# Kernel tuning notes

Measured on AMD Instinct MI355X. Metric: run time of the kernel, lower is better.

## Reference

```python
import jax, jax.numpy as jnp
import numpy as np

Q = 128      # number of slices
S = 8        # slice_length = C // Q = 1024 // 128
H = 32       # unit_dim[0]
BN_EPS = 1e-3  # Keras BatchNormalization default epsilon


def setup_inputs() -> dict:
    key = jax.random.key(0)
    ks = jax.random.split(key, 5)
    B = 32768
    x = jax.random.normal(ks[0], (B, 1, 1, Q * S), dtype=jnp.float32)
    # Per-slice (grouped) parameters for the q=128 independent MLPs.
    W1 = jax.random.normal(ks[1], (Q, S, H), dtype=jnp.float32) / np.sqrt(S)
    b1 = jnp.zeros((Q, H), dtype=jnp.float32)
    gamma = jnp.ones((Q, H), dtype=jnp.float32)
    beta = jnp.zeros((Q, H), dtype=jnp.float32)
    mov_mean = 0.1 * jax.random.normal(ks[2], (Q, H), dtype=jnp.float32)
    mov_var = jnp.ones((Q, H), dtype=jnp.float32) + 0.1 * jax.random.uniform(ks[3], (Q, H), dtype=jnp.float32)
    W2 = jax.random.normal(ks[4], (Q, H, 1), dtype=jnp.float32) / np.sqrt(H)
    b2 = jnp.zeros((Q, 1), dtype=jnp.float32)
    return {"x": x, "W1": W1, "b1": b1, "gamma": gamma, "beta": beta,
            "mov_mean": mov_mean, "mov_var": mov_var, "W2": W2, "b2": b2}


def reference(x, W1, b1, gamma, beta, mov_mean, mov_var, W2, b2):
    B = x.shape[0]
    xs = x.reshape(B, Q, -1)                       # (B, Q, S)
    # Grouped Dense(32) + ELU, all 128 slices in one batched matmul
    h = jnp.einsum('bqs,qsh->bqh', xs, W1) + b1    # (B, Q, H)
    h = jax.nn.elu(h)
    # BatchNormalization (inference: moving statistics)
    inv = gamma * jax.lax.rsqrt(mov_var + BN_EPS)  # (Q, H)
    h = (h - mov_mean) * inv + beta
    # Grouped Dense(1)
    out = jnp.einsum('bqh,qho->bqo', h, W2) + b2   # (B, Q, 1)
    return out[..., 0]                              # (B, Q)
```

## Files before the change

kernel.cpp:

```cpp
#include <hip/hip_runtime.h>
#include <hip/hip_bf16.h>


#define QN 128
#define SN 8
#define HN 32
#define XROW 1024
#define BN_EPS 1e-3f

typedef short bf16x8 __attribute__((ext_vector_type(8)));
typedef float f32x16 __attribute__((ext_vector_type(16)));
typedef unsigned int u32;

#define WS_A_BYTES (QN * 64 * 16)
#define WS_C_OFF   WS_A_BYTES
#define WS_C_BYTES (QN * 32 * 4)
#define WS_W_OFF   (WS_C_OFF + WS_C_BYTES)
#define WS_W_BYTES (QN * 32 * 4)
#define WS_B2_OFF  (WS_W_OFF + WS_W_BYTES)

static __device__ __forceinline__ u32 pkbf(float lo, float hi) {
    union { __hip_bfloat162 h2; u32 u; } c;
    c.h2 = __float22bfloat162_rn(float2{lo, hi});
    return c.u;
}

__global__ void divenc_prep(const float* __restrict__ W1, const float* __restrict__ b1,
                            const float* __restrict__ gamma_, const float* __restrict__ beta_,
                            const float* __restrict__ mmean, const float* __restrict__ mvar,
                            const float* __restrict__ W2, const float* __restrict__ b2,
                            unsigned char* __restrict__ ws)
{
    const int q = blockIdx.x;
    const int m = threadIdx.x;

    u32 d0 = 0, d1 = 0, d2 = 0, d3 = 0;
    if (m < 32) {
        d0 = pkbf(W1[(q*SN + 0)*HN + m], W1[(q*SN + 1)*HN + m]);
        d1 = pkbf(W1[(q*SN + 2)*HN + m], W1[(q*SN + 3)*HN + m]);
        d2 = pkbf(W1[(q*SN + 4)*HN + m], W1[(q*SN + 5)*HN + m]);
        d3 = pkbf(W1[(q*SN + 6)*HN + m], W1[(q*SN + 7)*HN + m]);
    }
    ((uint4*)ws)[q*64 + m] = uint4{d0, d1, d2, d3};

    float* wsC  = (float*)(ws + WS_C_OFF);
    float* wsW  = (float*)(ws + WS_W_OFF);
    float* wsB2 = (float*)(ws + WS_B2_OFF);
    if (m < 32) {
        const int half = m >> 4, r = m & 15;
        const int h = (r & 3) + 8*(r >> 2) + 4*half;
        wsC[q*32 + m] = b1[q*HN + h];
        float inv = gamma_[q*HN+h] * rsqrtf(mvar[q*HN+h] + BN_EPS);
        wsW[q*32 + m] = inv * W2[q*HN + h];
    }
    if (m == 0) {
        float acc = b2[q];
        for (int h = 0; h < HN; ++h) {
            float inv = gamma_[q*HN+h] * rsqrtf(mvar[q*HN+h] + BN_EPS);
            acc += (beta_[q*HN+h] - mmean[q*HN+h]*inv) * W2[q*HN+h];
        }
        wsB2[q] = acc;
    }
}

__global__ __launch_bounds__(512, 4)
void divenc_mfma(const float* __restrict__ x, const unsigned char* __restrict__ ws,
                 float* __restrict__ out)
{
    const int lane = threadIdx.x & 63;
    const int wv   = threadIdx.x >> 6;
    const int half = lane >> 5;
    const int bl   = lane & 31;
    const int b0   = blockIdx.x * 128;
    const int q0   = blockIdx.y * 32;

    const uint4* wsA  = (const uint4*)ws;
    const float* wsC  = (const float*)(ws + WS_C_OFF);
    const float* wsW  = (const float*)(ws + WS_W_OFF);
    const float* wsB2 = (const float*)(ws + WS_B2_OFF);

    __shared__ float slab[2][128][9];

    #pragma unroll
    for (int qg = 0; qg < 4; ++qg) {
        const int q = q0 + qg*8 + wv;

        union { uint4 u; bf16x8 v; } A1, A2;
        A1.u = wsA[q*64 + lane];
        A2.u = wsA[q*64 + (lane ^ 32)];

        f32x16 cini;
        const float* cp_ = wsC + q*32 + half*16;
        #pragma unroll
        for (int r = 0; r < 16; ++r) cini[r] = cp_[r];
        float w2r[16];
        const float* wp_ = wsW + q*32 + half*16;
        #pragma unroll
        for (int r = 0; r < 16; ++r) w2r[r] = wp_[r];
        const float b2p = wsB2[q];

        const float* xq = x + (size_t)b0 * XROW + q * SN;
        float4 xa = *(const float4*)(xq + (size_t)lane * XROW);
        float4 xc = *(const float4*)(xq + (size_t)lane * XROW + 4);

        #pragma unroll
        for (int sub = 0; sub < 2; ++sub) {
            const int nsub = (sub < 1) ? sub + 1 : sub;
            const float* np = xq + (size_t)(nsub*64 + lane) * XROW;
            float4 na = *(const float4*)np;
            float4 nc = *(const float4*)(np + 4);

            union { uint4 u; bf16x8 v; } B;
            B.u = uint4{ pkbf(xa.x, xa.y), pkbf(xa.z, xa.w),
                         pkbf(xc.x, xc.y), pkbf(xc.z, xc.w) };

            f32x16 D0 = __builtin_amdgcn_mfma_f32_32x32x16_bf16(A1.v, B.v, cini, 0, 0, 0);
            f32x16 D1 = __builtin_amdgcn_mfma_f32_32x32x16_bf16(A2.v, B.v, cini, 0, 0, 0);

            float p0 = 0.f, p1 = 0.f;
            #pragma unroll
            for (int r = 0; r < 16; ++r) {
                float z0 = D0[r];
                float e0 = __expf(fminf(z0, 0.f)) - 1.f;
                p0 = fmaf(fmaxf(z0, e0), w2r[r], p0);
                float z1 = D1[r];
                float e1 = __expf(fminf(z1, 0.f)) - 1.f;
                p1 = fmaf(fmaxf(z1, e1), w2r[r], p1);
            }
            p0 += __shfl_xor(p0, 32);
            p1 += __shfl_xor(p1, 32);

            const float v = (half ? p1 : p0) + b2p;
            slab[qg & 1][sub*64 + half*32 + bl][wv] = v;

            xa = na; xc = nc;
        }

        __syncthreads();
        {
            const int row = threadIdx.x >> 2;
            const int cp  = (threadIdx.x & 3) * 2;
            float2 vv;
            vv.x = slab[qg & 1][row][cp + 0];
            vv.y = slab[qg & 1][row][cp + 1];
            *(float2*)(out + (size_t)(b0 + row) * QN + q0 + qg*8 + cp) = vv;
        }
    }
}

extern "C" void kernel_launch(void* const* d_in, const int* in_sizes, int n_in,
                              void* d_out, int out_size, void* d_ws, size_t ws_size,
                              hipStream_t stream) {
    const float* x      = (const float*)d_in[0];
    const float* W1     = (const float*)d_in[1];
    const float* b1     = (const float*)d_in[2];
    const float* gamma_ = (const float*)d_in[3];
    const float* beta_  = (const float*)d_in[4];
    const float* mmean  = (const float*)d_in[5];
    const float* mvar   = (const float*)d_in[6];
    const float* W2     = (const float*)d_in[7];
    const float* b2     = (const float*)d_in[8];
    float* out = (float*)d_out;
    unsigned char* ws = (unsigned char*)d_ws;

    const int Btot = in_sizes[0] / XROW;

    divenc_prep<<<QN, 64, 0, stream>>>(W1, b1, gamma_, beta_, mmean, mvar, W2, b2, ws);
    divenc_mfma<<<dim3(Btot / 128, QN / 32), 512, 0, stream>>>(x, ws, out);
}
```

Before: 58.49 us.

## Stage x tiles into LDS with async double-buffered global_load_lds and swizzle

The kernel now copies x into shared memory with global_load_lds in 32-row chunks, double-buffered so the next chunk loads while the current one is computed. Each row segment covers 16 slices (512 contiguous bytes), so reads are coalesced instead of 32-byte strided per-lane loads. An XOR swizzle keeps LDS reads free of bank conflicts. Each wave now issues one MFMA per slice rather than two, and the grid uses 16 slices per block, doubling the block count. The risks are barrier overhead per chunk and relying on the compiler to wait for the LDS DMA to finish before the barrier.

```diff
diff --git a/kernel.cpp b/kernel.cpp
--- a/kernel.cpp
+++ b/kernel.cpp
@@ -7,10 +7,15 @@
 #define HN 32
 #define XROW 1024
 #define BN_EPS 1e-3f
+#define ROWS_BLK 128
+#define QBLK 16
 
 typedef short bf16x8 __attribute__((ext_vector_type(8)));
 typedef float f32x16 __attribute__((ext_vector_type(16)));
 typedef unsigned int u32;
+
+typedef __attribute__((address_space(1))) void as1_void;
+typedef __attribute__((address_space(3))) void as3_void;
 
 #define WS_A_BYTES (QN * 64 * 16)
 #define WS_C_OFF   WS_A_BYTES
@@ -63,6 +68,21 @@
     }
 }
 
+__device__ __forceinline__
+void stage_chunk(const float* __restrict__ x, u32* lds_base,
+                 int b0, int q0, int c, int wv, int lane)
+{
+    #pragma unroll
+    for (int k = 0; k < 2; ++k) {
+        const int i  = wv * 2 + k;
+        const int r  = i * 2 + (lane >> 5);
+        const int jl = (lane & 31) ^ r;
+        const float* src = x + (size_t)(b0 + c * 32 + r) * XROW + q0 * SN + jl * 4;
+        u32* dst = lds_base + i * 256;
+        __builtin_amdgcn_global_load_lds((const as1_void*)src, (as3_void*)dst, 16, 0, 0);
+    }
+}
+
 __global__ __launch_bounds__(512, 4)
 void divenc_mfma(const float* __restrict__ x, const unsigned char* __restrict__ ws,
                  float* __restrict__ out)
@@ -70,80 +90,79 @@
     const int lane = threadIdx.x & 63;
     const int wv   = threadIdx.x >> 6;
     const int half = lane >> 5;
-    const int bl   = lane & 31;
-    const int b0   = blockIdx.x * 128;
-    const int q0   = blockIdx.y * 32;
+    const int rr   = lane & 31;
+    const int b0   = blockIdx.x * ROWS_BLK;
+    const int q0   = blockIdx.y * QBLK;
 
     const uint4* wsA  = (const uint4*)ws;
     const float* wsC  = (const float*)(ws + WS_C_OFF);
     const float* wsW  = (const float*)(ws + WS_W_OFF);
     const float* wsB2 = (const float*)(ws + WS_B2_OFF);
 
-    __shared__ float slab[2][128][9];
+    __shared__ u32   xbuf[2][32 * 128];
+    __shared__ float slab[32][17];
 
-    #pragma unroll
-    for (int qg = 0; qg < 4; ++qg) {
-        const int q = q0 + qg*8 + wv;
+    stage_chunk(x, xbuf[0], b0, q0, 0, wv, lane);
 
-        union { uint4 u; bf16x8 v; } A1, A2;
-        A1.u = wsA[q*64 + lane];
-        A2.u = wsA[q*64 + (lane ^ 32)];
+    #pragma unroll 1
+    for (int c = 0; c < 4; ++c) {
+        __syncthreads();
 
-        f32x16 cini;
-        const float* cp_ = wsC + q*32 + half*16;
+        if (c < 3) stage_chunk(x, xbuf[(c + 1) & 1], b0, q0, c + 1, wv, lane);
+
+        const u32* xb = xbuf[c & 1];
         #pragma unroll
-        for (int r = 0; r < 16; ++r) cini[r] = cp_[r];
-        float w2r[16];
-        const float* wp_ = wsW + q*32 + half*16;
-        #pragma unroll
-        for (int r = 0; r < 16; ++r) w2r[r] = wp_[r];
-        const float b2p = wsB2[q];
+        for (int qg = 0; qg < 2; ++qg) {
+            const int ql = qg * 8 + wv;
+            const int q  = q0 + ql;
 
-        const float* xq = x + (size_t)b0 * XROW + q * SN;
-        float4 xa = *(const float4*)(xq + (size_t)lane * XROW);
-        float4 xc = *(const float4*)(xq + (size_t)lane * XROW + 4);
+            union { uint4 u; bf16x8 v; } A;
+            A.u = wsA[q * 64 + lane];
 
-        #pragma unroll
-        for (int sub = 0; sub < 2; ++sub) {
-            const int nsub = (sub < 1) ? sub + 1 : sub;
-            const float* np = xq + (size_t)(nsub*64 + lane) * XROW;
-            float4 na = *(const float4*)np;
-            float4 nc = *(const float4*)(np + 4);
+            f32x16 cini;
+            const float* cp_ = wsC + q * 32 + half * 16;
+            #pragma unroll
+            for (int r = 0; r < 16; ++r) cini[r] = cp_[r];
+            float w2r[16];
+            const float* wp_ = wsW + q * 32 + half * 16;
+            #pragma unroll
+            for (int r = 0; r < 16; ++r) w2r[r] = wp_[r];
+            const float b2p = wsB2[q];
+
+            const u32* rowp = xb + rr * 128;
+            const uint4 xw0 = *(const uint4*)(rowp + ((2 * ql)     ^ rr) * 4);
+            const uint4 xw1 = *(const uint4*)(rowp + ((2 * ql + 1) ^ rr) * 4);
 
             union { uint4 u; bf16x8 v; } B;
-            B.u = uint4{ pkbf(xa.x, xa.y), pkbf(xa.z, xa.w),
-                         pkbf(xc.x, xc.y), pkbf(xc.z, xc.w) };
+            B.u = uint4{ pkbf(__uint_as_float(xw0.x), __uint_as_float(xw0.y)),
+                         pkbf(__uint_as_float(xw0.z), __uint_as_float(xw0.w)),
+                         pkbf(__uint_as_float(xw1.x), __uint_as_float(xw1.y)),
+                         pkbf(__uint_as_float(xw1.z), __uint_as_float(xw1.w)) };
 
-            f32x16 D0 = __builtin_amdgcn_mfma_f32_32x32x16_bf16(A1.v, B.v, cini, 0, 0, 0);
-            f32x16 D1 = __builtin_amdgcn_mfma_f32_32x32x16_bf16(A2.v, B.v, cini, 0, 0, 0);
+            f32x16 D = __builtin_amdgcn_mfma_f32_32x32x16_bf16(A.v, B.v, cini, 0, 0, 0);
 
-            float p0 = 0.f, p1 = 0.f;
+            float p = 0.f;
             #pragma unroll
             for (int r = 0; r < 16; ++r) {
-                float z0 = D0[r];
-                float e0 = __expf(fminf(z0, 0.f)) - 1.f;
-                p0 = fmaf(fmaxf(z0, e0), w2r[r], p0);
-                float z1 = D1[r];
-                float e1 = __expf(fminf(z1, 0.f)) - 1.f;
-                p1 = fmaf(fmaxf(z1, e1), w2r[r], p1);
+                float z = D[r];
+                float e = __expf(fminf(z, 0.f)) - 1.f;
+                p = fmaf(fmaxf(z, e), w2r[r], p);
             }
-            p0 += __shfl_xor(p0, 32);
-            p1 += __shfl_xor(p1, 32);
-
-            const float v = (half ? p1 : p0) + b2p;
-            slab[qg & 1][sub*64 + half*32 + bl][wv] = v;
-
-            xa = na; xc = nc;
+            p += __shfl_xor(p, 32);
+            if (half == 0) slab[rr][ql] = p + b2p;
         }
 
         __syncthreads();
-        {
+
+        if (threadIdx.x < 128) {
             const int row = threadIdx.x >> 2;
-            const int cp  = (threadIdx.x & 3) * 2;
-            float2 vv;
-            vv.x = slab[qg & 1][row][cp + 0];
-            vv.y = slab[qg & 1][row][cp + 1];
-            *(float2*)(out + (size_t)(b0 + row) * QN + q0 + qg*8 + cp) = vv;
+            const int c4  = (threadIdx.x & 3) * 4;
+            float4 vv;
+            vv.x = slab[row][c4 + 0];
+            vv.y = slab[row][c4 + 1];
+            vv.z = slab[row][c4 + 2];
+            vv.w = slab[row][c4 + 3];
+            *(float4*)(out + (size_t)(b0 + c * 32 + row) * QN + q0 + c4) = vv;
         }
     }
 }
@@ -166,5 +185,5 @@
     const int Btot = in_sizes[0] / XROW;
 
     divenc_prep<<<QN, 64, 0, stream>>>(W1, b1, gamma_, beta_, mmean, mvar, W2, b2, ws);
-    divenc_mfma<<<dim3(Btot / 128, QN / 32), 512, 0, stream>>>(x, ws, out);
+    divenc_mfma<<<dim3(Btot / ROWS_BLK, QN / QBLK), 512, 0, stream>>>(x, ws, out);
 }
```

After: 61.58 us. 1.05x slower.

## Fold bias into MFMA K-padding, scalarize BN weights, single output write phase

Applied to the files above, without the earlier changes.

The bias b1 is folded into the zero-padded upper half of the K dimension, so a single 32x32x16 MFMA per 32-row sub-tile replaces two MFMAs with a loaded C initializer. Each MFMA now covers 32 batch rows instead of 64, so the ELU work is no longer done twice per tile, but the sub-tile count doubles to four. The folded BN/W2 weights are made wave-uniform through readfirstlane so they can sit in scalar registers. Output staging moves to a single 128x33 LDS slab with one barrier and float4 stores at the end, and the occupancy hint rises to 6. The risks are that half the lanes load x but discard it, and that the x prefetch double-buffering has been removed.

```diff
diff --git a/kernel.cpp b/kernel.cpp
--- a/kernel.cpp
+++ b/kernel.cpp
@@ -13,9 +13,7 @@
 typedef unsigned int u32;
 
 #define WS_A_BYTES (QN * 64 * 16)
-#define WS_C_OFF   WS_A_BYTES
-#define WS_C_BYTES (QN * 32 * 4)
-#define WS_W_OFF   (WS_C_OFF + WS_C_BYTES)
+#define WS_W_OFF   WS_A_BYTES
 #define WS_W_BYTES (QN * 32 * 4)
 #define WS_B2_OFF  (WS_W_OFF + WS_W_BYTES)
 
@@ -23,6 +21,9 @@
     union { __hip_bfloat162 h2; u32 u; } c;
     c.h2 = __float22bfloat162_rn(float2{lo, hi});
     return c.u;
+}
+static __device__ __forceinline__ float rfl(float v) {
+    return __uint_as_float(__builtin_amdgcn_readfirstlane(__float_as_uint(v)));
 }
 
 __global__ void divenc_prep(const float* __restrict__ W1, const float* __restrict__ b1,
@@ -40,16 +41,16 @@
         d1 = pkbf(W1[(q*SN + 2)*HN + m], W1[(q*SN + 3)*HN + m]);
         d2 = pkbf(W1[(q*SN + 4)*HN + m], W1[(q*SN + 5)*HN + m]);
         d3 = pkbf(W1[(q*SN + 6)*HN + m], W1[(q*SN + 7)*HN + m]);
+    } else {
+        d0 = pkbf(b1[q*HN + (m - 32)], 0.f);
     }
     ((uint4*)ws)[q*64 + m] = uint4{d0, d1, d2, d3};
 
-    float* wsC  = (float*)(ws + WS_C_OFF);
     float* wsW  = (float*)(ws + WS_W_OFF);
     float* wsB2 = (float*)(ws + WS_B2_OFF);
     if (m < 32) {
         const int half = m >> 4, r = m & 15;
         const int h = (r & 3) + 8*(r >> 2) + 4*half;
-        wsC[q*32 + m] = b1[q*HN + h];
         float inv = gamma_[q*HN+h] * rsqrtf(mvar[q*HN+h] + BN_EPS);
         wsW[q*32 + m] = inv * W2[q*HN + h];
     }
@@ -63,88 +64,91 @@
     }
 }
 
-__global__ __launch_bounds__(512, 4)
+__global__ __launch_bounds__(512, 6)
 void divenc_mfma(const float* __restrict__ x, const unsigned char* __restrict__ ws,
                  float* __restrict__ out)
 {
-    const int lane = threadIdx.x & 63;
-    const int wv   = threadIdx.x >> 6;
-    const int half = lane >> 5;
+    const int tid  = threadIdx.x;
+    const int lane = tid & 63;
+    const int wv   = __builtin_amdgcn_readfirstlane(tid >> 6);
     const int bl   = lane & 31;
+    const bool hi  = lane >= 32;
     const int b0   = blockIdx.x * 128;
     const int q0   = blockIdx.y * 32;
 
     const uint4* wsA  = (const uint4*)ws;
-    const float* wsC  = (const float*)(ws + WS_C_OFF);
     const float* wsW  = (const float*)(ws + WS_W_OFF);
     const float* wsB2 = (const float*)(ws + WS_B2_OFF);
 
-    __shared__ float slab[2][128][9];
+    __shared__ float slab[128][33];
 
     #pragma unroll
     for (int qg = 0; qg < 4; ++qg) {
         const int q = q0 + qg*8 + wv;
 
-        union { uint4 u; bf16x8 v; } A1, A2;
-        A1.u = wsA[q*64 + lane];
-        A2.u = wsA[q*64 + (lane ^ 32)];
+        union { uint4 u; bf16x8 v; } A;
+        A.u = wsA[q*64 + lane];
 
-        f32x16 cini;
-        const float* cp_ = wsC + q*32 + half*16;
+        const float* wp = wsW + q*32;
+        float sw[32];
         #pragma unroll
-        for (int r = 0; r < 16; ++r) cini[r] = cp_[r];
-        float w2r[16];
-        const float* wp_ = wsW + q*32 + half*16;
-        #pragma unroll
-        for (int r = 0; r < 16; ++r) w2r[r] = wp_[r];
-        const float b2p = wsB2[q];
+        for (int r = 0; r < 32; ++r) sw[r] = rfl(wp[r]);
+        const float b2p = rfl(wsB2[q]);
 
-        const float* xq = x + (size_t)b0 * XROW + q * SN;
-        float4 xa = *(const float4*)(xq + (size_t)lane * XROW);
-        float4 xc = *(const float4*)(xq + (size_t)lane * XROW + 4);
+        const float* xq = x + (size_t)(b0 + bl) * XROW + q * SN;
 
         #pragma unroll
-        for (int sub = 0; sub < 2; ++sub) {
-            const int nsub = (sub < 1) ? sub + 1 : sub;
-            const float* np = xq + (size_t)(nsub*64 + lane) * XROW;
-            float4 na = *(const float4*)np;
-            float4 nc = *(const float4*)(np + 4);
+        for (int sub = 0; sub < 4; ++sub) {
+            const float* xp = xq + (size_t)(sub * 32) * XROW;
+            float4 xa = *(const float4*)xp;
+            float4 xc = *(const float4*)(xp + 4);
+
+            const u32 k0 = pkbf(xa.x, xa.y), k1 = pkbf(xa.z, xa.w);
+            const u32 k2 = pkbf(xc.x, xc.y), k3 = pkbf(xc.z, xc.w);
 
             union { uint4 u; bf16x8 v; } B;
-            B.u = uint4{ pkbf(xa.x, xa.y), pkbf(xa.z, xa.w),
-                         pkbf(xc.x, xc.y), pkbf(xc.z, xc.w) };
+            B.u = uint4{ hi ? 0x00003F80u : k0,
+                         hi ? 0u : k1,
+                         hi ? 0u : k2,
+                         hi ? 0u : k3 };
 
-            f32x16 D0 = __builtin_amdgcn_mfma_f32_32x32x16_bf16(A1.v, B.v, cini, 0, 0, 0);
-            f32x16 D1 = __builtin_amdgcn_mfma_f32_32x32x16_bf16(A2.v, B.v, cini, 0, 0, 0);
+            f32x16 Z = {0.f,0.f,0.f,0.f,0.f,0.f,0.f,0.f,
+                        0.f,0.f,0.f,0.f,0.f,0.f,0.f,0.f};
+            f32x16 D = __builtin_amdgcn_mfma_f32_32x32x16_bf16(A.v, B.v, Z, 0, 0, 0);
 
-            float p0 = 0.f, p1 = 0.f;
+            float u_[16];
             #pragma unroll
             for (int r = 0; r < 16; ++r) {
-                float z0 = D0[r];
-                float e0 = __expf(fminf(z0, 0.f)) - 1.f;
-                p0 = fmaf(fmaxf(z0, e0), w2r[r], p0);
-                float z1 = D1[r];
-                float e1 = __expf(fminf(z1, 0.f)) - 1.f;
-                p1 = fmaf(fmaxf(z1, e1), w2r[r], p1);
+                float z = D[r];
+                float e = __expf(fminf(z, 0.f)) - 1.f;
+                u_[r] = fmaxf(z, e);
             }
-            p0 += __shfl_xor(p0, 32);
-            p1 += __shfl_xor(p1, 32);
+            float p = 0.f;
+            if (!hi) {
+                #pragma unroll
+                for (int r = 0; r < 16; ++r) p = fmaf(u_[r], sw[r], p);
+            } else {
+                #pragma unroll
+                for (int r = 0; r < 16; ++r) p = fmaf(u_[r], sw[16 + r], p);
+            }
+            p += __shfl_xor(p, 32);
+            if (!hi) slab[sub*32 + bl][qg*8 + wv] = p + b2p;
+        }
+    }
 
-            const float v = (half ? p1 : p0) + b2p;
-            slab[qg & 1][sub*64 + half*32 + bl][wv] = v;
+    __syncthreads();
 
-            xa = na; xc = nc;
-        }
-
-        __syncthreads();
-        {
-            const int row = threadIdx.x >> 2;
-            const int cp  = (threadIdx.x & 3) * 2;
-            float2 vv;
-            vv.x = slab[qg & 1][row][cp + 0];
-            vv.y = slab[qg & 1][row][cp + 1];
-            *(float2*)(out + (size_t)(b0 + row) * QN + q0 + qg*8 + cp) = vv;
-        }
+    {
+        const int row = tid >> 2;
+        const int c0  = (tid & 3) * 8;
+        float* orow = out + (size_t)(b0 + row) * QN + q0 + c0;
+        float4 v0, v1;
+        v0.x = slab[row][c0+0]; v0.y = slab[row][c0+1];
+        v0.z = slab[row][c0+2]; v0.w = slab[row][c0+3];
+        v1.x = slab[row][c0+4]; v1.y = slab[row][c0+5];
+        v1.z = slab[row][c0+6]; v1.w = slab[row][c0+7];
+        *(float4*)orow       = v0;
+        *(float4*)(orow + 4) = v1;
     }
 }
 
```

After: 55.58 us. 5.0% less time.
